# Optimization experiments

Measured on AMD Instinct MI355X. Metric: run time of the kernel, lower is better.

## Reference

```python
import jax, jax.numpy as jnp
import numpy as np

EPS = 1e-12  # matches torch F.normalize default eps

def _l2_normalize(x):
    n = jnp.maximum(jnp.linalg.norm(x, axis=-1, keepdims=True), EPS)
    return x / n

def setup_inputs() -> dict:
    key = jax.random.key(0)
    ks = jax.random.split(key, 6)
    B, H, N, D, E = 4, 12, 4096, 64, 32
    Q = jax.random.normal(ks[0], (B, H, N, D), dtype=jnp.float32)
    K = jax.random.normal(ks[1], (B, H, N, D), dtype=jnp.float32)
    we = jax.random.normal(ks[2], (2, H, D, E), dtype=jnp.float32)
    wr = jax.random.normal(ks[3], (2, H, D, E), dtype=jnp.float32)
    mask = jnp.ones((B, N), dtype=jnp.float32)
    W = jax.random.normal(ks[4], (D, 2 * E), dtype=jnp.float32) * (1.0 / np.sqrt(2 * E))
    b = jnp.zeros((D,), dtype=jnp.float32)
    Lambda = jax.random.uniform(ks[5], (H, E), dtype=jnp.float32)
    return {"Q": Q, "K": K, "we": we, "wr": wr, "mask": mask, "W": W, "b": b, "Lambda": Lambda}

def reference(Q, K, we, wr, mask, W, b, Lambda):
    # feature map: L2 normalize along head_dim
    queries = _l2_normalize(Q)   # [B,H,N,D]
    keys = _l2_normalize(K)      # [B,H,N,D]
    # per-head low-rank projections
    escore = jnp.einsum('bhnd,hde->bhne', queries, we[0])  # [B,H,N,E]
    rscore = jnp.einsum('bhnd,hde->bhne', keys, wr[0])     # [B,H,N,E]
    score = jnp.concatenate([escore, rscore], axis=-1)      # [B,H,N,2E]
    # Linear(2E -> D): score @ W.T + b
    attn_out = jnp.einsum('bhne,de->bhnd', score, W) + b
    attn_out = attn_out * mask[:, None, :, None]
    # trace_no_x = False branch
    return (attn_out, escore, rscore, we[0], wr[0], queries, keys, Lambda)
```

## Files before the change

### kernel.cpp

```cpp
#include <hip/hip_runtime.h>


namespace {
constexpr int Hh = 12;
constexpr int Nn = 4096;
constexpr int Dd = 64;
constexpr int O_ATTN = 0;
constexpr int O_ES   = 12582912;
constexpr int O_RS   = 18874368;
constexpr int O_WE   = 25165824;
constexpr int O_WR   = 25190400;
constexpr int O_Q    = 25214976;
constexpr int O_K    = 37797888;
constexpr int O_LAM  = 50380800;
}

typedef float  v4f  __attribute__((ext_vector_type(4)));
typedef __bf16 v8bf __attribute__((ext_vector_type(8)));

__device__ __forceinline__ unsigned short f2b(float f) {
    unsigned int x = __float_as_uint(f);
    x += 0x7fffu + ((x >> 16) & 1u);
    return (unsigned short)(x >> 16);
}

__device__ __forceinline__ int swz(int row, int k) {
    return row * 64 + (((k >> 3) ^ (row & 7)) << 3) + (k & 7);
}

__global__ __launch_bounds__(256, 4)
void pca_fused(const float* __restrict__ Q, const float* __restrict__ Kp,
               const float* __restrict__ we, const float* __restrict__ wr,
               const float* __restrict__ mask, const float* __restrict__ W,
               const float* __restrict__ bias, const float* __restrict__ Lam,
               float* __restrict__ out)
{
    __shared__ __align__(16) unsigned short Qs[4096];
    __shared__ __align__(16) unsigned short Ks[4096];
    __shared__ __align__(16) unsigned short WEs[2048];
    __shared__ __align__(16) unsigned short WRs[2048];
    __shared__ __align__(16) unsigned short Ws_[4096];

    const int tid = threadIdx.x;
    const int bh  = blockIdx.x >> 6;
    const int n0  = (blockIdx.x & 63) << 6;
    const int h   = bh % Hh;
    const int bb  = bh / Hh;

    if (blockIdx.x < 49) {
        int i4 = blockIdx.x * 256 + tid;
        if (i4 < 6144) {
            ((float4*)(out + O_WE))[i4] = ((const float4*)we)[i4];
        } else if (i4 < 12288) {
            ((float4*)(out + O_WR))[i4 - 6144] = ((const float4*)wr)[i4 - 6144];
        } else if (i4 < 12384) {
            ((float4*)(out + O_LAM))[i4 - 12288] = ((const float4*)Lam)[i4 - 12288];
        }
    }

    {
        const float* weh = we + h * 2048;
        const float* wrh = wr + h * 2048;
#pragma unroll
        for (int j = 0; j < 8; ++j) {
            int i = tid + 256 * j;
            int d = i >> 5, e = i & 31;
            WEs[swz(e, d)] = f2b(weh[i]);
            WRs[swz(e, d)] = f2b(wrh[i]);
        }
#pragma unroll
        for (int j = 0; j < 16; ++j) {
            int i = tid + 256 * j;
            int d = i >> 6, e = i & 63;
            Ws_[swz(d, e)] = f2b(W[i]);
        }
    }

    {
        const int rr = tid >> 4;
        const int c4 = (tid & 15) << 2;
#pragma unroll
        for (int p = 0; p < 4; ++p) {
            int r = p * 16 + rr;
            int g = (bh * Nn + n0 + r) * Dd + c4;
            float4 q4 = *(const float4*)(Q + g);
            float4 k4 = *(const float4*)(Kp + g);
            float sq = q4.x*q4.x + q4.y*q4.y + q4.z*q4.z + q4.w*q4.w;
            float sk = k4.x*k4.x + k4.y*k4.y + k4.z*k4.z + k4.w*k4.w;
#pragma unroll
            for (int m = 1; m < 16; m <<= 1) {
                sq += __shfl_xor(sq, m, 64);
                sk += __shfl_xor(sk, m, 64);
            }
            float iq = 1.0f / fmaxf(sqrtf(sq), 1e-12f);
            float ik = 1.0f / fmaxf(sqrtf(sk), 1e-12f);
            q4.x *= iq; q4.y *= iq; q4.z *= iq; q4.w *= iq;
            k4.x *= ik; k4.y *= ik; k4.z *= ik; k4.w *= ik;
            *(float4*)(out + O_Q + g) = q4;
            *(float4*)(out + O_K + g) = k4;
            int a = swz(r, c4);
            *(ushort4*)(Qs + a) = make_ushort4(f2b(q4.x), f2b(q4.y), f2b(q4.z), f2b(q4.w));
            *(ushort4*)(Ks + a) = make_ushort4(f2b(k4.x), f2b(k4.y), f2b(k4.z), f2b(k4.w));
        }
    }
    __syncthreads();

    const int w    = tid >> 6;
    const int lane = tid & 63;
    const int quad = lane >> 4;
    const int n16  = lane & 15;
    const int m    = w * 16 + n16;

    auto ldf = [&](const unsigned short* b, int row, int kb) -> v8bf {
        return *(const v8bf*)(b + row * 64 + ((((kb << 2) + quad) ^ (row & 7)) << 3));
    };

    v8bf aq0 = ldf(Qs, m, 0), aq1 = ldf(Qs, m, 1);
    v8bf ak0 = ldf(Ks, m, 0), ak1 = ldf(Ks, m, 1);
    v4f accE[2], accR[2];
#pragma unroll
    for (int nt = 0; nt < 2; ++nt) {
        int er = nt * 16 + n16;
        accE[nt] = (v4f){0.f, 0.f, 0.f, 0.f};
        accR[nt] = (v4f){0.f, 0.f, 0.f, 0.f};
        accE[nt] = __builtin_amdgcn_mfma_f32_16x16x32_bf16(aq0, ldf(WEs, er, 0), accE[nt], 0, 0, 0);
        accE[nt] = __builtin_amdgcn_mfma_f32_16x16x32_bf16(aq1, ldf(WEs, er, 1), accE[nt], 0, 0, 0);
        accR[nt] = __builtin_amdgcn_mfma_f32_16x16x32_bf16(ak0, ldf(WRs, er, 0), accR[nt], 0, 0, 0);
        accR[nt] = __builtin_amdgcn_mfma_f32_16x16x32_bf16(ak1, ldf(WRs, er, 1), accR[nt], 0, 0, 0);
    }

#pragma unroll
    for (int nt = 0; nt < 2; ++nt) {
#pragma unroll
        for (int i = 0; i < 4; ++i) {
            int r = w * 16 + quad * 4 + i;
            int n = n0 + r;
            out[O_ES + (bh * Nn + n) * 32 + nt * 16 + n16] = accE[nt][i];
            out[O_RS + (bh * Nn + n) * 32 + nt * 16 + n16] = accR[nt][i];
            Qs[swz(r, nt * 16 + n16)]      = f2b(accE[nt][i]);
            Qs[swz(r, 32 + nt * 16 + n16)] = f2b(accR[nt][i]);
        }
    }

    v8bf as0 = ldf(Qs, m, 0), as1 = ldf(Qs, m, 1);
    v4f accD[4];
#pragma unroll
    for (int nt = 0; nt < 4; ++nt) {
        float bv = bias[nt * 16 + n16];
        accD[nt] = (v4f){bv, bv, bv, bv};
        accD[nt] = __builtin_amdgcn_mfma_f32_16x16x32_bf16(as0, ldf(Ws_, nt * 16 + n16, 0), accD[nt], 0, 0, 0);
        accD[nt] = __builtin_amdgcn_mfma_f32_16x16x32_bf16(as1, ldf(Ws_, nt * 16 + n16, 1), accD[nt], 0, 0, 0);
    }
    float mv[4];
#pragma unroll
    for (int i = 0; i < 4; ++i) mv[i] = mask[bb * Nn + n0 + w * 16 + quad * 4 + i];
#pragma unroll
    for (int nt = 0; nt < 4; ++nt) {
#pragma unroll
        for (int i = 0; i < 4; ++i) {
            int n = n0 + w * 16 + quad * 4 + i;
            out[O_ATTN + (bh * Nn + n) * 64 + nt * 16 + n16] = accD[nt][i] * mv[i];
        }
    }
}

extern "C" void kernel_launch(void* const* d_in, const int* in_sizes, int n_in,
                              void* d_out, int out_size, void* d_ws, size_t ws_size,
                              hipStream_t stream) {
    const float* Q    = (const float*)d_in[0];
    const float* Kp   = (const float*)d_in[1];
    const float* we   = (const float*)d_in[2];
    const float* wr   = (const float*)d_in[3];
    const float* mask = (const float*)d_in[4];
    const float* W    = (const float*)d_in[5];
    const float* bias = (const float*)d_in[6];
    const float* Lam  = (const float*)d_in[7];
    float* out = (float*)d_out;

    pca_fused<<<dim3(48 * 64), dim3(256), 0, stream>>>(Q, Kp, we, wr, mask, W, bias, Lam, out);
}
```

Baseline: 302.0 us.

## Process four row tiles per block with register prefetch and hoisted weights

Shrinks the grid by 4x so each block loops over four 64-row tiles of one (b,h) slice. The per-head weights are converted to bf16 once per block and held in registers for every tile. The next tile's Q/K float4 loads are issued before the current tile's MFMA and store work, to hide global latency. In exchange there are fewer blocks, a lower occupancy hint (launch bounds 3), an extra barrier per tile, and higher register pressure.

```diff
diff --git a/kernel.cpp b/kernel.cpp
--- a/kernel.cpp
+++ b/kernel.cpp
@@ -4,7 +4,7 @@
 namespace {
 constexpr int Hh = 12;
 constexpr int Nn = 4096;
-constexpr int Dd = 64;
+constexpr int TPB = 4;
 constexpr int O_ATTN = 0;
 constexpr int O_ES   = 12582912;
 constexpr int O_RS   = 18874368;
@@ -28,7 +28,7 @@
     return row * 64 + (((k >> 3) ^ (row & 7)) << 3) + (k & 7);
 }
 
-__global__ __launch_bounds__(256, 4)
+__global__ __launch_bounds__(256, 3)
 void pca_fused(const float* __restrict__ Q, const float* __restrict__ Kp,
                const float* __restrict__ we, const float* __restrict__ wr,
                const float* __restrict__ mask, const float* __restrict__ W,
@@ -42,8 +42,8 @@
     __shared__ __align__(16) unsigned short Ws_[4096];
 
     const int tid = threadIdx.x;
-    const int bh  = blockIdx.x >> 6;
-    const int n0  = (blockIdx.x & 63) << 6;
+    const int bh  = blockIdx.x >> 4;
+    const int tb  = blockIdx.x & 15;
     const int h   = bh % Hh;
     const int bb  = bh / Hh;
 
@@ -76,21 +76,62 @@
         }
     }
 
+    const int rr = tid >> 4;
+    const int c4 = (tid & 15) << 2;
+
+    float4 pq[4], pk[4];
     {
-        const int rr = tid >> 4;
-        const int c4 = (tid & 15) << 2;
+        int g0 = (bh * Nn + (tb << 8)) * 64 + rr * 64 + c4;
+#pragma unroll
+        for (int p = 0; p < 4; ++p) {
+            pq[p] = *(const float4*)(Q  + g0 + p * 1024);
+            pk[p] = *(const float4*)(Kp + g0 + p * 1024);
+        }
+    }
+    __syncthreads();
+
+    const int w    = tid >> 6;
+    const int lane = tid & 63;
+    const int quad = lane >> 4;
+    const int n16  = lane & 15;
+    const int m    = w * 16 + n16;
+
+    auto ldf = [&](const unsigned short* b, int row, int kb) -> v8bf {
+        return *(const v8bf*)(b + row * 64 + ((((kb << 2) + quad) ^ (row & 7)) << 3));
+    };
+
+    v8bf wE[4], wR[4], wW[8];
+#pragma unroll
+    for (int nt = 0; nt < 2; ++nt) {
+        wE[nt * 2 + 0] = ldf(WEs, nt * 16 + n16, 0);
+        wE[nt * 2 + 1] = ldf(WEs, nt * 16 + n16, 1);
+        wR[nt * 2 + 0] = ldf(WRs, nt * 16 + n16, 0);
+        wR[nt * 2 + 1] = ldf(WRs, nt * 16 + n16, 1);
+    }
+#pragma unroll
+    for (int nt = 0; nt < 4; ++nt) {
+        wW[nt * 2 + 0] = ldf(Ws_, nt * 16 + n16, 0);
+        wW[nt * 2 + 1] = ldf(Ws_, nt * 16 + n16, 1);
+    }
+    float bv4[4];
+#pragma unroll
+    for (int nt = 0; nt < 4; ++nt) bv4[nt] = bias[nt * 16 + n16];
+
+    for (int it = 0; it < TPB; ++it) {
+        const int n0 = ((tb << 2) + it) << 6;
+        const int gt = (bh * Nn + n0) * 64;
+
 #pragma unroll
         for (int p = 0; p < 4; ++p) {
             int r = p * 16 + rr;
-            int g = (bh * Nn + n0 + r) * Dd + c4;
-            float4 q4 = *(const float4*)(Q + g);
-            float4 k4 = *(const float4*)(Kp + g);
+            int g = gt + r * 64 + c4;
+            float4 q4 = pq[p], k4 = pk[p];
             float sq = q4.x*q4.x + q4.y*q4.y + q4.z*q4.z + q4.w*q4.w;
             float sk = k4.x*k4.x + k4.y*k4.y + k4.z*k4.z + k4.w*k4.w;
 #pragma unroll
-            for (int m = 1; m < 16; m <<= 1) {
-                sq += __shfl_xor(sq, m, 64);
-                sk += __shfl_xor(sk, m, 64);
+            for (int mm = 1; mm < 16; mm <<= 1) {
+                sq += __shfl_xor(sq, mm, 64);
+                sk += __shfl_xor(sk, mm, 64);
             }
             float iq = 1.0f / fmaxf(sqrtf(sq), 1e-12f);
             float ik = 1.0f / fmaxf(sqrtf(sk), 1e-12f);
@@ -102,64 +143,63 @@
             *(ushort4*)(Qs + a) = make_ushort4(f2b(q4.x), f2b(q4.y), f2b(q4.z), f2b(q4.w));
             *(ushort4*)(Ks + a) = make_ushort4(f2b(k4.x), f2b(k4.y), f2b(k4.z), f2b(k4.w));
         }
-    }
-    __syncthreads();
-
-    const int w    = tid >> 6;
-    const int lane = tid & 63;
-    const int quad = lane >> 4;
-    const int n16  = lane & 15;
-    const int m    = w * 16 + n16;
-
-    auto ldf = [&](const unsigned short* b, int row, int kb) -> v8bf {
-        return *(const v8bf*)(b + row * 64 + ((((kb << 2) + quad) ^ (row & 7)) << 3));
-    };
-
-    v8bf aq0 = ldf(Qs, m, 0), aq1 = ldf(Qs, m, 1);
-    v8bf ak0 = ldf(Ks, m, 0), ak1 = ldf(Ks, m, 1);
-    v4f accE[2], accR[2];
-#pragma unroll
-    for (int nt = 0; nt < 2; ++nt) {
-        int er = nt * 16 + n16;
-        accE[nt] = (v4f){0.f, 0.f, 0.f, 0.f};
-        accR[nt] = (v4f){0.f, 0.f, 0.f, 0.f};
-        accE[nt] = __builtin_amdgcn_mfma_f32_16x16x32_bf16(aq0, ldf(WEs, er, 0), accE[nt], 0, 0, 0);
-        accE[nt] = __builtin_amdgcn_mfma_f32_16x16x32_bf16(aq1, ldf(WEs, er, 1), accE[nt], 0, 0, 0);
-        accR[nt] = __builtin_amdgcn_mfma_f32_16x16x32_bf16(ak0, ldf(WRs, er, 0), accR[nt], 0, 0, 0);
-        accR[nt] = __builtin_amdgcn_mfma_f32_16x16x32_bf16(ak1, ldf(WRs, er, 1), accR[nt], 0, 0, 0);
-    }
-
-#pragma unroll
-    for (int nt = 0; nt < 2; ++nt) {
-#pragma unroll
-        for (int i = 0; i < 4; ++i) {
-            int r = w * 16 + quad * 4 + i;
-            int n = n0 + r;
-            out[O_ES + (bh * Nn + n) * 32 + nt * 16 + n16] = accE[nt][i];
-            out[O_RS + (bh * Nn + n) * 32 + nt * 16 + n16] = accR[nt][i];
-            Qs[swz(r, nt * 16 + n16)]      = f2b(accE[nt][i]);
-            Qs[swz(r, 32 + nt * 16 + n16)] = f2b(accR[nt][i]);
-        }
-    }
-
-    v8bf as0 = ldf(Qs, m, 0), as1 = ldf(Qs, m, 1);
-    v4f accD[4];
-#pragma unroll
-    for (int nt = 0; nt < 4; ++nt) {
-        float bv = bias[nt * 16 + n16];
-        accD[nt] = (v4f){bv, bv, bv, bv};
-        accD[nt] = __builtin_amdgcn_mfma_f32_16x16x32_bf16(as0, ldf(Ws_, nt * 16 + n16, 0), accD[nt], 0, 0, 0);
-        accD[nt] = __builtin_amdgcn_mfma_f32_16x16x32_bf16(as1, ldf(Ws_, nt * 16 + n16, 1), accD[nt], 0, 0, 0);
-    }
-    float mv[4];
-#pragma unroll
-    for (int i = 0; i < 4; ++i) mv[i] = mask[bb * Nn + n0 + w * 16 + quad * 4 + i];
-#pragma unroll
-    for (int nt = 0; nt < 4; ++nt) {
-#pragma unroll
-        for (int i = 0; i < 4; ++i) {
-            int n = n0 + w * 16 + quad * 4 + i;
-            out[O_ATTN + (bh * Nn + n) * 64 + nt * 16 + n16] = accD[nt][i] * mv[i];
+        if (it + 1 < TPB) {
+            int gn = gt + 64 * 64 + rr * 64 + c4;
+#pragma unroll
+            for (int p = 0; p < 4; ++p) {
+                pq[p] = *(const float4*)(Q  + gn + p * 1024);
+                pk[p] = *(const float4*)(Kp + gn + p * 1024);
+            }
+        }
+        __syncthreads();
+
+        v8bf aq0 = ldf(Qs, m, 0), aq1 = ldf(Qs, m, 1);
+        v8bf ak0 = ldf(Ks, m, 0), ak1 = ldf(Ks, m, 1);
+        v4f accE[2], accR[2];
+#pragma unroll
+        for (int nt = 0; nt < 2; ++nt) {
+            accE[nt] = (v4f){0.f, 0.f, 0.f, 0.f};
+            accR[nt] = (v4f){0.f, 0.f, 0.f, 0.f};
+            accE[nt] = __builtin_amdgcn_mfma_f32_16x16x32_bf16(aq0, wE[nt*2+0], accE[nt], 0, 0, 0);
+            accE[nt] = __builtin_amdgcn_mfma_f32_16x16x32_bf16(aq1, wE[nt*2+1], accE[nt], 0, 0, 0);
+            accR[nt] = __builtin_amdgcn_mfma_f32_16x16x32_bf16(ak0, wR[nt*2+0], accR[nt], 0, 0, 0);
+            accR[nt] = __builtin_amdgcn_mfma_f32_16x16x32_bf16(ak1, wR[nt*2+1], accR[nt], 0, 0, 0);
+        }
+
+#pragma unroll
+        for (int nt = 0; nt < 2; ++nt) {
+#pragma unroll
+            for (int i = 0; i < 4; ++i) {
+                int r = w * 16 + quad * 4 + i;
+                int n = n0 + r;
+                out[O_ES + (bh * Nn + n) * 32 + nt * 16 + n16] = accE[nt][i];
+                out[O_RS + (bh * Nn + n) * 32 + nt * 16 + n16] = accR[nt][i];
+                Qs[swz(r, nt * 16 + n16)]      = f2b(accE[nt][i]);
+                Qs[swz(r, 32 + nt * 16 + n16)] = f2b(accR[nt][i]);
+            }
+        }
+
+        v8bf as0 = ldf(Qs, m, 0), as1 = ldf(Qs, m, 1);
+        v4f accD[4];
+#pragma unroll
+        for (int nt = 0; nt < 4; ++nt) {
+            float bv = bv4[nt];
+            accD[nt] = (v4f){bv, bv, bv, bv};
+            accD[nt] = __builtin_amdgcn_mfma_f32_16x16x32_bf16(as0, wW[nt*2+0], accD[nt], 0, 0, 0);
+            accD[nt] = __builtin_amdgcn_mfma_f32_16x16x32_bf16(as1, wW[nt*2+1], accD[nt], 0, 0, 0);
+        }
+        __syncthreads();
+
+        float mv[4];
+#pragma unroll
+        for (int i = 0; i < 4; ++i) mv[i] = mask[bb * Nn + n0 + w * 16 + quad * 4 + i];
+#pragma unroll
+        for (int nt = 0; nt < 4; ++nt) {
+#pragma unroll
+            for (int i = 0; i < 4; ++i) {
+                int n = n0 + w * 16 + quad * 4 + i;
+                out[O_ATTN + (bh * Nn + n) * 64 + nt * 16 + n16] = accD[nt][i] * mv[i];
+            }
         }
     }
 }
@@ -177,5 +217,5 @@
     const float* Lam  = (const float*)d_in[7];
     float* out = (float*)d_out;
 
-    pca_fused<<<dim3(48 * 64), dim3(256), 0, stream>>>(Q, Kp, we, wr, mask, W, bias, Lam, out);
-}
+    pca_fused<<<dim3(48 * 16), dim3(256), 0, stream>>>(Q, Kp, we, wr, mask, W, bias, Lam, out);
+}
```

Measured after the change: 320.1 us. 6.0% more time.

## Persistent per-wave slab loop with register prefetch of next Q/K tiles

Applied to the files above, without the earlier changes.

Each block now processes 256 rows in four iterations instead of 64 rows once, with each wave owning a private 16-row slab in LDS. The weight conversion into LDS is amortized over four times as many rows. Q/K for the next iteration are prefetched into registers while the current slab is normalized and run through MFMA. Per-wave LDS buffers mean the block-wide barrier is needed only once. The trade-offs are fewer blocks (768) for latency hiding, more registers, and a larger LDS footprint.

```diff
diff --git a/kernel.cpp b/kernel.cpp
--- a/kernel.cpp
+++ b/kernel.cpp
@@ -4,7 +4,6 @@
 namespace {
 constexpr int Hh = 12;
 constexpr int Nn = 4096;
-constexpr int Dd = 64;
 constexpr int O_ATTN = 0;
 constexpr int O_ES   = 12582912;
 constexpr int O_RS   = 18874368;
@@ -35,15 +34,16 @@
                const float* __restrict__ bias, const float* __restrict__ Lam,
                float* __restrict__ out)
 {
-    __shared__ __align__(16) unsigned short Qs[4096];
-    __shared__ __align__(16) unsigned short Ks[4096];
     __shared__ __align__(16) unsigned short WEs[2048];
     __shared__ __align__(16) unsigned short WRs[2048];
     __shared__ __align__(16) unsigned short Ws_[4096];
+    __shared__ __align__(16) unsigned short Qsl[4096];
+    __shared__ __align__(16) unsigned short Ksl[4096];
+    __shared__ __align__(16) unsigned short Ssl[4096];
 
     const int tid = threadIdx.x;
-    const int bh  = blockIdx.x >> 6;
-    const int n0  = (blockIdx.x & 63) << 6;
+    const int bh  = blockIdx.x >> 4;
+    const int tb  = blockIdx.x & 15;
     const int h   = bh % Hh;
     const int bb  = bh / Hh;
 
@@ -76,90 +76,124 @@
         }
     }
 
+    const int w    = tid >> 6;
+    const int lane = tid & 63;
+    const int quad = lane >> 4;
+    const int n16  = lane & 15;
+    unsigned short* Qs = Qsl + w * 1024;
+    unsigned short* Ks = Ksl + w * 1024;
+    unsigned short* Ss = Ssl + w * 1024;
+
+    const int lr = lane >> 4;
+    const int lc = (lane & 15) << 2;
+
+    auto slab_base = [&](int it) {
+        return tb * 256 + it * 64 + w * 16;
+    };
+
+    float4 pq[4], pk[4];
     {
-        const int rr = tid >> 4;
-        const int c4 = (tid & 15) << 2;
+        int g0 = (bh * Nn + slab_base(0) + lr) * 64 + lc;
 #pragma unroll
         for (int p = 0; p < 4; ++p) {
-            int r = p * 16 + rr;
-            int g = (bh * Nn + n0 + r) * Dd + c4;
-            float4 q4 = *(const float4*)(Q + g);
-            float4 k4 = *(const float4*)(Kp + g);
+            pq[p] = *(const float4*)(Q  + g0 + p * 256);
+            pk[p] = *(const float4*)(Kp + g0 + p * 256);
+        }
+    }
+
+    auto ldf = [&](const unsigned short* b, int row, int kb) -> v8bf {
+        return *(const v8bf*)(b + row * 64 + ((((kb << 2) + quad) ^ (row & 7)) << 3));
+    };
+
+    float bv4[4];
+#pragma unroll
+    for (int nt = 0; nt < 4; ++nt) bv4[nt] = bias[nt * 16 + n16];
+
+    __syncthreads();
+
+    for (int it = 0; it < 4; ++it) {
+        const int nb = slab_base(it);
+        const int gt = (bh * Nn + nb) * 64;
+
+#pragma unroll
+        for (int p = 0; p < 4; ++p) {
+            int r = p * 4 + lr;
+            float4 q4 = pq[p], k4 = pk[p];
             float sq = q4.x*q4.x + q4.y*q4.y + q4.z*q4.z + q4.w*q4.w;
             float sk = k4.x*k4.x + k4.y*k4.y + k4.z*k4.z + k4.w*k4.w;
 #pragma unroll
-            for (int m = 1; m < 16; m <<= 1) {
-                sq += __shfl_xor(sq, m, 64);
-                sk += __shfl_xor(sk, m, 64);
+            for (int mm = 1; mm < 16; mm <<= 1) {
+                sq += __shfl_xor(sq, mm, 64);
+                sk += __shfl_xor(sk, mm, 64);
             }
             float iq = 1.0f / fmaxf(sqrtf(sq), 1e-12f);
             float ik = 1.0f / fmaxf(sqrtf(sk), 1e-12f);
             q4.x *= iq; q4.y *= iq; q4.z *= iq; q4.w *= iq;
             k4.x *= ik; k4.y *= ik; k4.z *= ik; k4.w *= ik;
+            int g = gt + r * 64 + lc;
             *(float4*)(out + O_Q + g) = q4;
             *(float4*)(out + O_K + g) = k4;
-            int a = swz(r, c4);
+            int a = swz(r, lc);
             *(ushort4*)(Qs + a) = make_ushort4(f2b(q4.x), f2b(q4.y), f2b(q4.z), f2b(q4.w));
             *(ushort4*)(Ks + a) = make_ushort4(f2b(k4.x), f2b(k4.y), f2b(k4.z), f2b(k4.w));
         }
-    }
-    __syncthreads();
-
-    const int w    = tid >> 6;
-    const int lane = tid & 63;
-    const int quad = lane >> 4;
-    const int n16  = lane & 15;
-    const int m    = w * 16 + n16;
-
-    auto ldf = [&](const unsigned short* b, int row, int kb) -> v8bf {
-        return *(const v8bf*)(b + row * 64 + ((((kb << 2) + quad) ^ (row & 7)) << 3));
-    };
-
-    v8bf aq0 = ldf(Qs, m, 0), aq1 = ldf(Qs, m, 1);
-    v8bf ak0 = ldf(Ks, m, 0), ak1 = ldf(Ks, m, 1);
-    v4f accE[2], accR[2];
-#pragma unroll
-    for (int nt = 0; nt < 2; ++nt) {
-        int er = nt * 16 + n16;
-        accE[nt] = (v4f){0.f, 0.f, 0.f, 0.f};
-        accR[nt] = (v4f){0.f, 0.f, 0.f, 0.f};
-        accE[nt] = __builtin_amdgcn_mfma_f32_16x16x32_bf16(aq0, ldf(WEs, er, 0), accE[nt], 0, 0, 0);
-        accE[nt] = __builtin_amdgcn_mfma_f32_16x16x32_bf16(aq1, ldf(WEs, er, 1), accE[nt], 0, 0, 0);
-        accR[nt] = __builtin_amdgcn_mfma_f32_16x16x32_bf16(ak0, ldf(WRs, er, 0), accR[nt], 0, 0, 0);
-        accR[nt] = __builtin_amdgcn_mfma_f32_16x16x32_bf16(ak1, ldf(WRs, er, 1), accR[nt], 0, 0, 0);
-    }
-
-#pragma unroll
-    for (int nt = 0; nt < 2; ++nt) {
-#pragma unroll
-        for (int i = 0; i < 4; ++i) {
-            int r = w * 16 + quad * 4 + i;
-            int n = n0 + r;
-            out[O_ES + (bh * Nn + n) * 32 + nt * 16 + n16] = accE[nt][i];
-            out[O_RS + (bh * Nn + n) * 32 + nt * 16 + n16] = accR[nt][i];
-            Qs[swz(r, nt * 16 + n16)]      = f2b(accE[nt][i]);
-            Qs[swz(r, 32 + nt * 16 + n16)] = f2b(accR[nt][i]);
-        }
-    }
-
-    v8bf as0 = ldf(Qs, m, 0), as1 = ldf(Qs, m, 1);
-    v4f accD[4];
-#pragma unroll
-    for (int nt = 0; nt < 4; ++nt) {
-        float bv = bias[nt * 16 + n16];
-        accD[nt] = (v4f){bv, bv, bv, bv};
-        accD[nt] = __builtin_amdgcn_mfma_f32_16x16x32_bf16(as0, ldf(Ws_, nt * 16 + n16, 0), accD[nt], 0, 0, 0);
-        accD[nt] = __builtin_amdgcn_mfma_f32_16x16x32_bf16(as1, ldf(Ws_, nt * 16 + n16, 1), accD[nt], 0, 0, 0);
-    }
-    float mv[4];
-#pragma unroll
-    for (int i = 0; i < 4; ++i) mv[i] = mask[bb * Nn + n0 + w * 16 + quad * 4 + i];
-#pragma unroll
-    for (int nt = 0; nt < 4; ++nt) {
-#pragma unroll
-        for (int i = 0; i < 4; ++i) {
-            int n = n0 + w * 16 + quad * 4 + i;
-            out[O_ATTN + (bh * Nn + n) * 64 + nt * 16 + n16] = accD[nt][i] * mv[i];
+
+        if (it + 1 < 4) {
+            int gn = (bh * Nn + slab_base(it + 1) + lr) * 64 + lc;
+#pragma unroll
+            for (int p = 0; p < 4; ++p) {
+                pq[p] = *(const float4*)(Q  + gn + p * 256);
+                pk[p] = *(const float4*)(Kp + gn + p * 256);
+            }
+        }
+
+        v8bf aq0 = ldf(Qs, n16, 0), aq1 = ldf(Qs, n16, 1);
+        v8bf ak0 = ldf(Ks, n16, 0), ak1 = ldf(Ks, n16, 1);
+        v4f accE[2], accR[2];
+#pragma unroll
+        for (int nt = 0; nt < 2; ++nt) {
+            int er = nt * 16 + n16;
+            accE[nt] = (v4f){0.f, 0.f, 0.f, 0.f};
+            accR[nt] = (v4f){0.f, 0.f, 0.f, 0.f};
+            accE[nt] = __builtin_amdgcn_mfma_f32_16x16x32_bf16(aq0, ldf(WEs, er, 0), accE[nt], 0, 0, 0);
+            accE[nt] = __builtin_amdgcn_mfma_f32_16x16x32_bf16(aq1, ldf(WEs, er, 1), accE[nt], 0, 0, 0);
+            accR[nt] = __builtin_amdgcn_mfma_f32_16x16x32_bf16(ak0, ldf(WRs, er, 0), accR[nt], 0, 0, 0);
+            accR[nt] = __builtin_amdgcn_mfma_f32_16x16x32_bf16(ak1, ldf(WRs, er, 1), accR[nt], 0, 0, 0);
+        }
+
+#pragma unroll
+        for (int nt = 0; nt < 2; ++nt) {
+#pragma unroll
+            for (int i = 0; i < 4; ++i) {
+                int r = quad * 4 + i;
+                int n = nb + r;
+                out[O_ES + (bh * Nn + n) * 32 + nt * 16 + n16] = accE[nt][i];
+                out[O_RS + (bh * Nn + n) * 32 + nt * 16 + n16] = accR[nt][i];
+                Ss[swz(r, nt * 16 + n16)]      = f2b(accE[nt][i]);
+                Ss[swz(r, 32 + nt * 16 + n16)] = f2b(accR[nt][i]);
+            }
+        }
+
+        v8bf as0 = ldf(Ss, n16, 0), as1 = ldf(Ss, n16, 1);
+        v4f accD[4];
+#pragma unroll
+        for (int nt = 0; nt < 4; ++nt) {
+            float bv = bv4[nt];
+            accD[nt] = (v4f){bv, bv, bv, bv};
+            accD[nt] = __builtin_amdgcn_mfma_f32_16x16x32_bf16(as0, ldf(Ws_, nt * 16 + n16, 0), accD[nt], 0, 0, 0);
+            accD[nt] = __builtin_amdgcn_mfma_f32_16x16x32_bf16(as1, ldf(Ws_, nt * 16 + n16, 1), accD[nt], 0, 0, 0);
+        }
+
+        float mv[4];
+#pragma unroll
+        for (int i = 0; i < 4; ++i) mv[i] = mask[bb * Nn + nb + quad * 4 + i];
+#pragma unroll
+        for (int nt = 0; nt < 4; ++nt) {
+#pragma unroll
+            for (int i = 0; i < 4; ++i) {
+                int n = nb + quad * 4 + i;
+                out[O_ATTN + (bh * Nn + n) * 64 + nt * 16 + n16] = accD[nt][i] * mv[i];
+            }
         }
     }
 }
@@ -177,5 +211,5 @@
     const float* Lam  = (const float*)d_in[7];
     float* out = (float*)d_out;
 
-    pca_fused<<<dim3(48 * 64), dim3(256), 0, stream>>>(Q, Kp, we, wr, mask, W, bias, Lam, out);
-}
+    pca_fused<<<dim3(48 * 16), dim3(256), 0, stream>>>(Q, Kp, we, wr, mask, W, bias, Lam, out);
+}
```

Result: slower. 348.4 us (+15.4%).
